# Optimization experiments

Measured on AMD Instinct MI355X. Metric: run time of the kernel, lower is better.

Reference implementation:

```python
import jax, jax.numpy as jnp
import numpy as np

TEMPERATURE = 0.07
EPS = 1e-8  # torch CosineSimilarity eps
N, D = 8192, 128

def setup_inputs() -> dict:
    key = jax.random.key(0)
    k1, k2, k3 = jax.random.split(key, 3)
    features = jax.random.normal(k1, (N, D), dtype=jnp.float32)
    positive_mask = jax.random.randint(k2, (N, N), 0, 2, dtype=jnp.int32)
    negative_mask = jax.random.randint(k3, (N, N), 0, 2, dtype=jnp.int32)
    return {"features": features, "positive_mask": positive_mask, "negative_mask": negative_mask}

def reference(features, positive_mask, negative_mask):
    n = positive_mask.shape[0]
    # remove self-contrast (zero the diagonal)
    not_self = 1.0 - jnp.eye(n, dtype=features.dtype)
    pos_m = positive_mask.astype(features.dtype) * not_self
    neg_m = negative_mask.astype(features.dtype) * not_self
    # cosine similarity: normalize once, then Gram matrix [N, N]
    norms = jnp.maximum(jnp.linalg.norm(features, axis=-1, keepdims=True), EPS)
    fn = features / norms
    sim = jnp.exp(jnp.einsum('id,jd->ij', fn, fn) / TEMPERATURE)  # [N, N]
    pos = jnp.sum(sim * pos_m, axis=1)
    neg = jnp.sum(sim * neg_m, axis=1)
    loss = -jnp.mean(jnp.log(pos / (pos + neg)))
    return loss
```

## Files before the change

kernel.cpp:

```cpp
#include <hip/hip_runtime.h>
#include <hip/hip_bf16.h>

#define N 8192
#define D 128
#define INV_T 14.285714285714286f
#define LDS_PITCH 136

typedef __bf16 v8bf __attribute__((ext_vector_type(8)));
typedef __bf16 v4bf __attribute__((ext_vector_type(4)));
typedef float  v4f  __attribute__((ext_vector_type(4)));

__global__ __launch_bounds__(256) void normalize_kernel(
    const float* __restrict__ f, __bf16* __restrict__ out)
{
    int gwave = (blockIdx.x * blockDim.x + threadIdx.x) >> 6;
    int lane  = threadIdx.x & 63;
    const float2 v = *reinterpret_cast<const float2*>(f + (size_t)gwave * D + lane * 2);
    float ss = v.x * v.x + v.y * v.y;
    #pragma unroll
    for (int m = 32; m; m >>= 1) ss += __shfl_xor(ss, m);
    float inv = 1.0f / fmaxf(sqrtf(ss), 1e-8f);
    __bf16* o = out + (size_t)gwave * D + lane * 2;
    o[0] = (__bf16)(v.x * inv);
    o[1] = (__bf16)(v.y * inv);
}

__global__ __launch_bounds__(256) void supcon_main(
    const __bf16* __restrict__ F,
    const int* __restrict__ pmask, const int* __restrict__ nmask,
    float* __restrict__ pos, float* __restrict__ neg)
{
    __shared__ __bf16 E[128 * LDS_PITCH];

    const int tid  = threadIdx.x;
    const int lane = tid & 63;
    const int wid  = tid >> 6;
    const int wr   = wid >> 1, wc = wid & 1;
    const int i0   = blockIdx.y * 128;
    const int j0   = blockIdx.x * 128;
    const int iw   = i0 + wr * 64;
    const int jw   = j0 + wc * 64;
    const int r    = lane & 15;
    const int q    = lane >> 4;

    v4f acc[4][4];
    #pragma unroll
    for (int m = 0; m < 4; ++m)
        #pragma unroll
        for (int n = 0; n < 4; ++n) acc[m][n] = (v4f)0.0f;

    #pragma unroll
    for (int ks = 0; ks < 4; ++ks) {
        v8bf a[4], b[4];
        #pragma unroll
        for (int m = 0; m < 4; ++m)
            a[m] = *reinterpret_cast<const v8bf*>(F + (size_t)(iw + m * 16 + r) * D + ks * 32 + q * 8);
        #pragma unroll
        for (int n = 0; n < 4; ++n)
            b[n] = *reinterpret_cast<const v8bf*>(F + (size_t)(jw + n * 16 + r) * D + ks * 32 + q * 8);
        #pragma unroll
        for (int m = 0; m < 4; ++m)
            #pragma unroll
            for (int n = 0; n < 4; ++n)
                acc[m][n] = __builtin_amdgcn_mfma_f32_16x16x32_bf16(a[m], b[n], acc[m][n], 0, 0, 0);
    }

    const bool diag = (blockIdx.x == blockIdx.y);
    #pragma unroll
    for (int m = 0; m < 4; ++m) {
        #pragma unroll
        for (int n = 0; n < 4; ++n) {
            const int colL = wc * 64 + n * 16 + r;
            #pragma unroll
            for (int v = 0; v < 4; ++v) {
                const int rowL = wr * 64 + m * 16 + q * 4 + v;
                float e = __expf(acc[m][n][v] * INV_T);
                if (diag && rowL == colL) e = 0.0f;
                E[rowL * LDS_PITCH + colL] = (__bf16)e;
            }
        }
    }
    __syncthreads();

    const int half = lane >> 5;
    const int c    = lane & 31;
    float pacc[16], gacc[16];
    #pragma unroll
    for (int it = 0; it < 16; ++it) {
        const int row = wid * 32 + it * 2 + half;
        const size_t base = (size_t)(i0 + row) * N + j0 + c * 4;
        const int4 pm = *reinterpret_cast<const int4*>(pmask + base);
        const int4 nm = *reinterpret_cast<const int4*>(nmask + base);
        const v4bf ev = *reinterpret_cast<const v4bf*>(&E[row * LDS_PITCH + c * 4]);
        const float e0 = (float)ev[0], e1 = (float)ev[1];
        const float e2 = (float)ev[2], e3 = (float)ev[3];
        pacc[it] = fmaf((float)pm.x, e0, fmaf((float)pm.y, e1,
                   fmaf((float)pm.z, e2, (float)pm.w * e3)));
        gacc[it] = fmaf((float)nm.x, e0, fmaf((float)nm.y, e1,
                   fmaf((float)nm.z, e2, (float)nm.w * e3)));
    }

    #pragma unroll
    for (int it = 0; it < 16; ++it) {
        float p = pacc[it], g = gacc[it];
        #pragma unroll
        for (int msk = 1; msk < 32; msk <<= 1) {
            p += __shfl_xor(p, msk);
            g += __shfl_xor(g, msk);
        }
        if (c == 0) {
            const int gi = i0 + wid * 32 + it * 2 + half;
            atomicAdd(&pos[gi], p);
            atomicAdd(&neg[gi], g);
        }
    }
}

__global__ __launch_bounds__(1024) void finalize_kernel(
    const float* __restrict__ pos, const float* __restrict__ neg, float* __restrict__ out)
{
    __shared__ float sm[16];
    int tid = threadIdx.x;
    float acc = 0.0f;
    for (int i = tid; i < N; i += 1024) {
        float p = pos[i], g = neg[i];
        acc += logf(p / (p + g));
    }
    #pragma unroll
    for (int m = 32; m; m >>= 1) acc += __shfl_xor(acc, m);
    if ((tid & 63) == 0) sm[tid >> 6] = acc;
    __syncthreads();
    if (tid == 0) {
        float t = 0.0f;
        #pragma unroll
        for (int w = 0; w < 16; ++w) t += sm[w];
        out[0] = -t * (1.0f / (float)N);
    }
}

extern "C" void kernel_launch(void* const* d_in, const int* in_sizes, int n_in,
                              void* d_out, int out_size, void* d_ws, size_t ws_size,
                              hipStream_t stream) {
    const float* feat  = (const float*)d_in[0];
    const int*   pmask = (const int*)d_in[1];
    const int*   nmask = (const int*)d_in[2];
    float* out = (float*)d_out;

    char* ws = (char*)d_ws;
    __bf16* fnb = (__bf16*)ws;
    float*  pos = (float*)(ws + (size_t)2 * 1024 * 1024);
    float*  neg = pos + N;

    hipMemsetAsync(pos, 0, 2 * N * sizeof(float), stream);

    normalize_kernel<<<dim3(N / 4), 256, 0, stream>>>(feat, fnb);

    dim3 grid(N / 128, N / 128);
    supcon_main<<<grid, 256, 0, stream>>>(fnb, pmask, nmask, pos, neg);

    finalize_kernel<<<1, 1024, 0, stream>>>(pos, neg, out);
}
```

Measured before the change: 587.6 us.

## Pre-pack int32 masks into bitmasks before the fused similarity kernel

Adds a streaming kernel that packs the two int32 N×N masks into 1-bit-per-entry bitmaps in the workspace. The main tile kernel then reads 4-byte bit words and selects exp values by bit test, instead of loading int4 masks and doing FMAs. The full 512 MB of masks is still read on every call, now in a separate bandwidth-bound pass. The intent is to let the mask read run as a simple coalesced stream and lighten the main kernel's memory traffic, at the cost of an extra launch and a 16 MB intermediate.

Result: slower. 661.6 us (+12.6%).

```diff
diff --git a/kernel.cpp b/kernel.cpp
--- a/kernel.cpp
+++ b/kernel.cpp
@@ -9,6 +9,31 @@
 typedef __bf16 v8bf __attribute__((ext_vector_type(8)));
 typedef __bf16 v4bf __attribute__((ext_vector_type(4)));
 typedef float  v4f  __attribute__((ext_vector_type(4)));
+
+__global__ __launch_bounds__(256) void pack_masks(
+    const int* __restrict__ pmask, const int* __restrict__ nmask,
+    unsigned char* __restrict__ pbits, unsigned char* __restrict__ nbits)
+{
+    const int nthreads = gridDim.x * blockDim.x;
+    const int total = N * N / 8;
+    for (int t = blockIdx.x * blockDim.x + threadIdx.x; t < total; t += nthreads) {
+        const size_t e = (size_t)t * 8;
+        const int4 a0 = *reinterpret_cast<const int4*>(pmask + e);
+        const int4 a1 = *reinterpret_cast<const int4*>(pmask + e + 4);
+        const int4 b0 = *reinterpret_cast<const int4*>(nmask + e);
+        const int4 b1 = *reinterpret_cast<const int4*>(nmask + e + 4);
+        unsigned pb = (unsigned)(a0.x != 0)        | ((unsigned)(a0.y != 0) << 1)
+                    | ((unsigned)(a0.z != 0) << 2) | ((unsigned)(a0.w != 0) << 3)
+                    | ((unsigned)(a1.x != 0) << 4) | ((unsigned)(a1.y != 0) << 5)
+                    | ((unsigned)(a1.z != 0) << 6) | ((unsigned)(a1.w != 0) << 7);
+        unsigned nb = (unsigned)(b0.x != 0)        | ((unsigned)(b0.y != 0) << 1)
+                    | ((unsigned)(b0.z != 0) << 2) | ((unsigned)(b0.w != 0) << 3)
+                    | ((unsigned)(b1.x != 0) << 4) | ((unsigned)(b1.y != 0) << 5)
+                    | ((unsigned)(b1.z != 0) << 6) | ((unsigned)(b1.w != 0) << 7);
+        pbits[t] = (unsigned char)pb;
+        nbits[t] = (unsigned char)nb;
+    }
+}
 
 __global__ __launch_bounds__(256) void normalize_kernel(
     const float* __restrict__ f, __bf16* __restrict__ out)
@@ -27,7 +52,7 @@
 
 __global__ __launch_bounds__(256) void supcon_main(
     const __bf16* __restrict__ F,
-    const int* __restrict__ pmask, const int* __restrict__ nmask,
+    const unsigned char* __restrict__ pbits, const unsigned char* __restrict__ nbits,
     float* __restrict__ pos, float* __restrict__ neg)
 {
     __shared__ __bf16 E[128 * LDS_PITCH];
@@ -84,20 +109,27 @@
 
     const int half = lane >> 5;
     const int c    = lane & 31;
+    const int row0 = wid * 32 + half;
+    const int wsel = (c >> 3) << 2;
+    const int nib  = (c & 7) * 4;
     float pacc[16], gacc[16];
+
     #pragma unroll
     for (int it = 0; it < 16; ++it) {
-        const int row = wid * 32 + it * 2 + half;
-        const size_t base = (size_t)(i0 + row) * N + j0 + c * 4;
-        const int4 pm = *reinterpret_cast<const int4*>(pmask + base);
-        const int4 nm = *reinterpret_cast<const int4*>(nmask + base);
+        const int row = row0 + 2 * it;
+        const int gi  = i0 + row;
+        const size_t bb = (size_t)gi * (N / 8) + (j0 >> 3) + wsel;
+        const unsigned pw = *reinterpret_cast<const unsigned*>(pbits + bb);
+        const unsigned nw = *reinterpret_cast<const unsigned*>(nbits + bb);
+        const unsigned pn = (pw >> nib) & 0xFu;
+        const unsigned nn = (nw >> nib) & 0xFu;
         const v4bf ev = *reinterpret_cast<const v4bf*>(&E[row * LDS_PITCH + c * 4]);
         const float e0 = (float)ev[0], e1 = (float)ev[1];
         const float e2 = (float)ev[2], e3 = (float)ev[3];
-        pacc[it] = fmaf((float)pm.x, e0, fmaf((float)pm.y, e1,
-                   fmaf((float)pm.z, e2, (float)pm.w * e3)));
-        gacc[it] = fmaf((float)nm.x, e0, fmaf((float)nm.y, e1,
-                   fmaf((float)nm.z, e2, (float)nm.w * e3)));
+        pacc[it] = ((pn & 1u) ? e0 : 0.0f) + ((pn & 2u) ? e1 : 0.0f)
+                 + ((pn & 4u) ? e2 : 0.0f) + ((pn & 8u) ? e3 : 0.0f);
+        gacc[it] = ((nn & 1u) ? e0 : 0.0f) + ((nn & 2u) ? e1 : 0.0f)
+                 + ((nn & 4u) ? e2 : 0.0f) + ((nn & 8u) ? e3 : 0.0f);
     }
 
     #pragma unroll
@@ -109,7 +141,7 @@
             g += __shfl_xor(g, msk);
         }
         if (c == 0) {
-            const int gi = i0 + wid * 32 + it * 2 + half;
+            const int gi = i0 + row0 + it * 2;
             atomicAdd(&pos[gi], p);
             atomicAdd(&neg[gi], g);
         }
@@ -150,13 +182,16 @@
     __bf16* fnb = (__bf16*)ws;
     float*  pos = (float*)(ws + (size_t)2 * 1024 * 1024);
     float*  neg = pos + N;
+    unsigned char* pbits = (unsigned char*)(ws + (size_t)4 * 1024 * 1024);
+    unsigned char* nbits = (unsigned char*)(ws + (size_t)12 * 1024 * 1024);
 
     hipMemsetAsync(pos, 0, 2 * N * sizeof(float), stream);
 
+    pack_masks<<<dim3(2048), 256, 0, stream>>>(pmask, nmask, pbits, nbits);
     normalize_kernel<<<dim3(N / 4), 256, 0, stream>>>(feat, fnb);
 
     dim3 grid(N / 128, N / 128);
-    supcon_main<<<grid, 256, 0, stream>>>(fnb, pmask, nmask, pos, neg);
+    supcon_main<<<grid, 256, 0, stream>>>(fnb, pbits, nbits, pos, neg);
 
     finalize_kernel<<<1, 1024, 0, stream>>>(pos, neg, out);
 }
```
